# Performance work log

Hardware: AMD Instinct MI355X
Metric: run time of the kernel (lower is better)

The kernel has to match this reference:

```python
import jax, jax.numpy as jnp
import numpy as np

B, A, G, C = 32, 3, 64, 80
MAXB = 50
IOU_THRESH = 0.5


def setup_inputs() -> dict:
    key = jax.random.key(0)
    k1, k2, k3, k4, k5, k6 = jax.random.split(key, 6)
    # predictions hold probabilities directly (log applied in BCE), keep in (0,1)
    predictions = jax.random.uniform(k1, (B, A, G, G, C + 5), jnp.float32, 0.01, 0.99)
    anchors = jnp.concatenate([
        jax.random.uniform(k2, (A, G, G, 2), jnp.float32, 0.0, 512.0),   # cx,cy
        jax.random.uniform(k3, (A, G, G, 2), jnp.float32, 16.0, 160.0),  # w,h
    ], axis=-1)
    cxcy = jax.random.uniform(k4, (B, MAXB, 2), jnp.float32, 0.0, 512.0)
    wh = jax.random.uniform(k5, (B, MAXB, 2), jnp.float32, 16.0, 160.0)
    cls = jax.random.randint(k6, (B, MAXB), 0, C).astype(jnp.float32)
    valid = jax.random.uniform(jax.random.fold_in(key, 7), (B, MAXB)) < 0.6
    cls = jnp.where(valid, cls, -1.0)
    bbox_annotations = jnp.concatenate([cxcy, wh, cls[..., None]], axis=-1)
    return {"predictions": predictions, "bbox_annotations": bbox_annotations,
            "anchors": anchors, "input_dim": 512, "num_classes": C,
            "num_anchors": A, "grid_size": G}


def _iou_xywh(a, b):
    # a: (N,4) (cx,cy,w,h); b: (M,4) -> (N,M) pairwise IoU
    ax1, ay1 = a[:, 0] - a[:, 2] / 2, a[:, 1] - a[:, 3] / 2
    ax2, ay2 = a[:, 0] + a[:, 2] / 2, a[:, 1] + a[:, 3] / 2
    bx1, by1 = b[:, 0] - b[:, 2] / 2, b[:, 1] - b[:, 3] / 2
    bx2, by2 = b[:, 0] + b[:, 2] / 2, b[:, 1] + b[:, 3] / 2
    iw = jnp.clip(jnp.minimum(ax2[:, None], bx2[None, :]) - jnp.maximum(ax1[:, None], bx1[None, :]), 0)
    ih = jnp.clip(jnp.minimum(ay2[:, None], by2[None, :]) - jnp.maximum(ay1[:, None], by1[None, :]), 0)
    inter = iw * ih
    area_a = (ax2 - ax1) * (ay2 - ay1)
    area_b = (bx2 - bx1) * (by2 - by1)
    return inter / jnp.clip(area_a[:, None] + area_b[None, :] - inter, 1e-8)


def _per_image(pred, ann, anchors_flat, num_classes, iou_thresh):
    cls_p = pred[..., 5:].reshape(-1, num_classes)  # (N, C)
    valid = ann[:, 4] != -1                          # (M,)
    ious = _iou_xywh(anchors_flat, ann[:, :4])       # (N, M)
    ious = jnp.where(valid[None, :], ious, -1.0)     # invalid anns never match
    ious_max = ious.max(axis=1)
    ious_argmax = ious.argmax(axis=1)
    positive = ious_max >= iou_thresh                # (N,)
    assigned_cls = jnp.clip(ann[ious_argmax, 4], 0, num_classes - 1).astype(jnp.int32)
    gt = jax.nn.one_hot(assigned_cls, num_classes, dtype=cls_p.dtype) * positive[:, None]
    bce = -(gt * jnp.log(cls_p) + (1.0 - gt) * jnp.log(1.0 - cls_p))
    num_pos = positive.sum()
    cls_loss = (bce * positive[:, None]).sum() / jnp.maximum(num_pos, 1).astype(cls_p.dtype)
    has_ann = valid.any()
    cls_loss = jnp.where(has_ann, cls_loss, 0.0)
    reg_loss = jnp.zeros((), cls_p.dtype)
    return cls_loss, reg_loss


def reference(predictions, bbox_annotations, anchors, input_dim, num_classes, num_anchors, grid_size):
    anchors_flat = anchors.reshape(-1, 4)  # (A*G*G, 4)
    cls_losses, reg_losses = jax.vmap(_per_image, in_axes=(0, 0, None, None, None))(
        predictions, bbox_annotations, anchors_flat, num_classes, IOU_THRESH)
    return jnp.stack([cls_losses, reg_losses])  # (2, B)
```

## Files before the change

### kernel.cpp

```cpp
#include <hip/hip_runtime.h>

#define BATCH   32
#define NCLS    80
#define MAXB    50
#define NANCH   12288
#define BLK     256
#define BLKS_PER_IMG 48
#define ROWLEN  85

__global__ __launch_bounds__(BLK) void yolo_match_bce(
    const float* __restrict__ pred,
    const float* __restrict__ ann,
    const float* __restrict__ anchors,
    float* __restrict__ psum,
    int*   __restrict__ pcnt)
{
    const int blk = blockIdx.x;
    const int b   = blockIdx.y;
    const int n   = blk * BLK + threadIdx.x;

    __shared__ float4 s_box[MAXB];
    __shared__ float  s_area[MAXB];
    __shared__ float  s_cls[MAXB];
    __shared__ int    s_nv;

    if (threadIdx.x < 64) {
        const int lane = threadIdx.x;
        float cx = 0, cy = 0, w = 0, h = 0, cl = -1.0f;
        if (lane < MAXB) {
            const float* a = ann + ((size_t)b * MAXB + lane) * 5;
            cx = a[0]; cy = a[1]; w = a[2]; h = a[3]; cl = a[4];
        }
        const bool valid = (lane < MAXB) && (cl != -1.0f);
        const unsigned long long mask = __ballot(valid);
        if (valid) {
            const int cidx = __popcll(mask & ((1ull << lane) - 1ull));
            const float x1 = cx - w * 0.5f, y1 = cy - h * 0.5f;
            const float x2 = cx + w * 0.5f, y2 = cy + h * 0.5f;
            s_box[cidx]  = make_float4(x1, y1, x2, y2);
            s_area[cidx] = (x2 - x1) * (y2 - y1);
            s_cls[cidx]  = cl;
        }
        if (lane == 0) s_nv = __popcll(mask);
    }
    __syncthreads();

    const float4 a4 = *reinterpret_cast<const float4*>(anchors + (size_t)n * 4);
    const float ax1 = a4.x - a4.z * 0.5f, ay1 = a4.y - a4.w * 0.5f;
    const float ax2 = a4.x + a4.z * 0.5f, ay2 = a4.y + a4.w * 0.5f;
    const float area_a = (ax2 - ax1) * (ay2 - ay1);

    const int nv = s_nv;
    float best = 0.0f;
    int   bestm = 0;
    #pragma unroll 5
    for (int m = 0; m < nv; ++m) {
        const float4 bb = s_box[m];
        float iw = fminf(ax2, bb.z) - fmaxf(ax1, bb.x); iw = fmaxf(iw, 0.0f);
        float ih = fminf(ay2, bb.w) - fmaxf(ay1, bb.y); ih = fmaxf(ih, 0.0f);
        const float inter = iw * ih;
        const float ua    = area_a + s_area[m] - inter;
        const float iou   = inter * __builtin_amdgcn_rcpf(ua);
        if (iou > best) { best = iou; bestm = m; }
    }

    const bool positive = (best >= 0.5f);
    float local = 0.0f;
    if (positive) {
        const int ac = (int)fminf(fmaxf(s_cls[bestm], 0.0f), (float)(NCLS - 1));
        const float* prow = pred + ((size_t)b * NANCH + n) * ROWLEN + 5;
        float S = 0.0f;
        #pragma unroll
        for (int ch = 0; ch < 5; ++ch) {
            float prod = 1.0f;
            #pragma unroll
            for (int j = 0; j < 16; ++j) {
                const float p = prow[ch * 16 + j];
                prod = __builtin_fmaf(-p, prod, prod);
            }
            S += __logf(prod);
        }
        const float pa = prow[ac];
        local = -__logf(pa) + __logf(1.0f - pa) - S;
    }

    float v = local;
    int   c = positive ? 1 : 0;
    #pragma unroll
    for (int off = 32; off > 0; off >>= 1) {
        v += __shfl_down(v, off, 64);
        c += __shfl_down(c, off, 64);
    }
    __shared__ float s_sum[BLK / 64];
    __shared__ int   s_cnt[BLK / 64];
    const int wave = threadIdx.x >> 6;
    if ((threadIdx.x & 63) == 0) { s_sum[wave] = v; s_cnt[wave] = c; }
    __syncthreads();
    if (threadIdx.x == 0) {
        float t = 0.0f; int tc = 0;
        #pragma unroll
        for (int w = 0; w < BLK / 64; ++w) { t += s_sum[w]; tc += s_cnt[w]; }
        psum[b * BLKS_PER_IMG + blk] = t;
        pcnt[b * BLKS_PER_IMG + blk] = tc;
    }
}

__global__ __launch_bounds__(64) void yolo_finalize(
    const float* __restrict__ psum,
    const int*   __restrict__ pcnt,
    float* __restrict__ out)
{
    const int b = blockIdx.x;
    const int t = threadIdx.x;
    float v = (t < BLKS_PER_IMG) ? psum[b * BLKS_PER_IMG + t] : 0.0f;
    int   c = (t < BLKS_PER_IMG) ? pcnt[b * BLKS_PER_IMG + t] : 0;
    #pragma unroll
    for (int off = 32; off > 0; off >>= 1) {
        v += __shfl_down(v, off, 64);
        c += __shfl_down(c, off, 64);
    }
    if (t == 0) {
        const int np = (c > 1) ? c : 1;
        out[b]         = v / (float)np;
        out[BATCH + b] = 0.0f;
    }
}

extern "C" void kernel_launch(void* const* d_in, const int* in_sizes, int n_in,
                              void* d_out, int out_size, void* d_ws, size_t ws_size,
                              hipStream_t stream) {
    const float* pred    = (const float*)d_in[0];
    const float* ann     = (const float*)d_in[1];
    const float* anchors = (const float*)d_in[2];
    float* out = (float*)d_out;

    float* psum = (float*)d_ws;
    int*   pcnt = (int*)((char*)d_ws + sizeof(float) * BATCH * BLKS_PER_IMG);

    dim3 grid1(BLKS_PER_IMG, BATCH);
    yolo_match_bce<<<grid1, BLK, 0, stream>>>(pred, ann, anchors, psum, pcnt);
    yolo_finalize<<<BATCH, 64, 0, stream>>>(psum, pcnt, out);
}
```

Measured before the change: 17.50 us.

## Fuse finalize into main kernel via packed atomic last-block reduction, two anchors per thread

Removes the separate finalize kernel. Each block atomically adds a packed 64-bit word holding a block counter, positive count and fixed-point sum, and the last block writes the per-image loss. Each thread now handles two anchors, which halves the grid and amortizes the shared annotation setup. In exchange it adds a memset launch and converts the sum to fixed point, which can lose precision or overflow the 44-bit field for large losses.

```diff
diff --git a/kernel.cpp b/kernel.cpp
--- a/kernel.cpp
+++ b/kernel.cpp
@@ -5,19 +5,23 @@
 #define MAXB    50
 #define NANCH   12288
 #define BLK     256
-#define BLKS_PER_IMG 48
+#define APT     2
+#define BLKS_PER_IMG (NANCH / (BLK * APT))
 #define ROWLEN  85
+#define SUM_SCALE 16384.0f
 
-__global__ __launch_bounds__(BLK) void yolo_match_bce(
+typedef unsigned long long u64;
+
+__global__ __launch_bounds__(BLK) void yolo_fused(
     const float* __restrict__ pred,
     const float* __restrict__ ann,
     const float* __restrict__ anchors,
-    float* __restrict__ psum,
-    int*   __restrict__ pcnt)
+    u64*         __restrict__ gpack,
+    float*       __restrict__ out)
 {
     const int blk = blockIdx.x;
     const int b   = blockIdx.y;
-    const int n   = blk * BLK + threadIdx.x;
+    const int n0  = blk * (BLK * APT) + threadIdx.x;
 
     __shared__ float4 s_box[MAXB];
     __shared__ float  s_area[MAXB];
@@ -32,7 +36,7 @@
             cx = a[0]; cy = a[1]; w = a[2]; h = a[3]; cl = a[4];
         }
         const bool valid = (lane < MAXB) && (cl != -1.0f);
-        const unsigned long long mask = __ballot(valid);
+        const u64 mask = __ballot(valid);
         if (valid) {
             const int cidx = __popcll(mask & ((1ull << lane) - 1ull));
             const float x1 = cx - w * 0.5f, y1 = cy - h * 0.5f;
@@ -45,47 +49,71 @@
     }
     __syncthreads();
 
-    const float4 a4 = *reinterpret_cast<const float4*>(anchors + (size_t)n * 4);
-    const float ax1 = a4.x - a4.z * 0.5f, ay1 = a4.y - a4.w * 0.5f;
-    const float ax2 = a4.x + a4.z * 0.5f, ay2 = a4.y + a4.w * 0.5f;
-    const float area_a = (ax2 - ax1) * (ay2 - ay1);
+    const float4 A0 = *reinterpret_cast<const float4*>(anchors + (size_t)n0 * 4);
+    const float4 A1 = *reinterpret_cast<const float4*>(anchors + (size_t)(n0 + BLK) * 4);
+    const float ax1_0 = A0.x - A0.z * 0.5f, ay1_0 = A0.y - A0.w * 0.5f;
+    const float ax2_0 = A0.x + A0.z * 0.5f, ay2_0 = A0.y + A0.w * 0.5f;
+    const float ax1_1 = A1.x - A1.z * 0.5f, ay1_1 = A1.y - A1.w * 0.5f;
+    const float ax2_1 = A1.x + A1.z * 0.5f, ay2_1 = A1.y + A1.w * 0.5f;
+    const float area0 = (ax2_0 - ax1_0) * (ay2_0 - ay1_0);
+    const float area1 = (ax2_1 - ax1_1) * (ay2_1 - ay1_1);
 
     const int nv = s_nv;
-    float best = 0.0f;
-    int   bestm = 0;
-    #pragma unroll 5
+    float best0 = 0.0f, best1 = 0.0f;
+    int   bm0 = 0, bm1 = 0;
+    #pragma unroll 2
     for (int m = 0; m < nv; ++m) {
         const float4 bb = s_box[m];
-        float iw = fminf(ax2, bb.z) - fmaxf(ax1, bb.x); iw = fmaxf(iw, 0.0f);
-        float ih = fminf(ay2, bb.w) - fmaxf(ay1, bb.y); ih = fmaxf(ih, 0.0f);
-        const float inter = iw * ih;
-        const float ua    = area_a + s_area[m] - inter;
-        const float iou   = inter * __builtin_amdgcn_rcpf(ua);
-        if (iou > best) { best = iou; bestm = m; }
+        const float ab  = s_area[m];
+        float iw0 = fminf(ax2_0, bb.z) - fmaxf(ax1_0, bb.x); iw0 = fmaxf(iw0, 0.0f);
+        float ih0 = fminf(ay2_0, bb.w) - fmaxf(ay1_0, bb.y); ih0 = fmaxf(ih0, 0.0f);
+        float iw1 = fminf(ax2_1, bb.z) - fmaxf(ax1_1, bb.x); iw1 = fmaxf(iw1, 0.0f);
+        float ih1 = fminf(ay2_1, bb.w) - fmaxf(ay1_1, bb.y); ih1 = fmaxf(ih1, 0.0f);
+        const float in0 = iw0 * ih0;
+        const float in1 = iw1 * ih1;
+        const float iou0 = in0 * __builtin_amdgcn_rcpf(area0 + ab - in0);
+        const float iou1 = in1 * __builtin_amdgcn_rcpf(area1 + ab - in1);
+        if (iou0 > best0) { best0 = iou0; bm0 = m; }
+        if (iou1 > best1) { best1 = iou1; bm1 = m; }
     }
 
-    const bool positive = (best >= 0.5f);
+    const bool pos0 = (best0 >= 0.5f);
+    const bool pos1 = (best1 >= 0.5f);
     float local = 0.0f;
-    if (positive) {
-        const int ac = (int)fminf(fmaxf(s_cls[bestm], 0.0f), (float)(NCLS - 1));
-        const float* prow = pred + ((size_t)b * NANCH + n) * ROWLEN + 5;
+
+    if (pos0) {
+        const int ac = (int)fminf(fmaxf(s_cls[bm0], 0.0f), (float)(NCLS - 1));
+        const float* prow = pred + ((size_t)b * NANCH + n0) * ROWLEN + 5;
         float S = 0.0f;
         #pragma unroll
         for (int ch = 0; ch < 5; ++ch) {
             float prod = 1.0f;
             #pragma unroll
-            for (int j = 0; j < 16; ++j) {
-                const float p = prow[ch * 16 + j];
-                prod = __builtin_fmaf(-p, prod, prod);
-            }
+            for (int j = 0; j < 16; ++j)
+                prod = __builtin_fmaf(-prow[ch * 16 + j], prod, prod);
             S += __logf(prod);
         }
         const float pa = prow[ac];
-        local = -__logf(pa) + __logf(1.0f - pa) - S;
+        local += -__logf(pa) + __logf(1.0f - pa) - S;
+    }
+    if (pos1) {
+        const int ac = (int)fminf(fmaxf(s_cls[bm1], 0.0f), (float)(NCLS - 1));
+        const float* prow = pred + ((size_t)b * NANCH + n0 + BLK) * ROWLEN + 5;
+        float S = 0.0f;
+        #pragma unroll
+        for (int ch = 0; ch < 5; ++ch) {
+            float prod = 1.0f;
+            #pragma unroll
+            for (int j = 0; j < 16; ++j)
+                prod = __builtin_fmaf(-prow[ch * 16 + j], prod, prod);
+            S += __logf(prod);
+        }
+        const float pa = prow[ac];
+        local += -__logf(pa) + __logf(1.0f - pa) - S;
     }
 
     float v = local;
-    int   c = positive ? 1 : 0;
+    int   c = (pos0 ? 1 : 0) + (pos1 ? 1 : 0);
     #pragma unroll
     for (int off = 32; off > 0; off >>= 1) {
         v += __shfl_down(v, off, 64);
@@ -96,33 +124,21 @@
     const int wave = threadIdx.x >> 6;
     if ((threadIdx.x & 63) == 0) { s_sum[wave] = v; s_cnt[wave] = c; }
     __syncthreads();
+
     if (threadIdx.x == 0) {
         float t = 0.0f; int tc = 0;
         #pragma unroll
         for (int w = 0; w < BLK / 64; ++w) { t += s_sum[w]; tc += s_cnt[w]; }
-        psum[b * BLKS_PER_IMG + blk] = t;
-        pcnt[b * BLKS_PER_IMG + blk] = tc;
-    }
-}
-
-__global__ __launch_bounds__(64) void yolo_finalize(
-    const float* __restrict__ psum,
-    const int*   __restrict__ pcnt,
-    float* __restrict__ out)
-{
-    const int b = blockIdx.x;
-    const int t = threadIdx.x;
-    float v = (t < BLKS_PER_IMG) ? psum[b * BLKS_PER_IMG + t] : 0.0f;
-    int   c = (t < BLKS_PER_IMG) ? pcnt[b * BLKS_PER_IMG + t] : 0;
-    #pragma unroll
-    for (int off = 32; off > 0; off >>= 1) {
-        v += __shfl_down(v, off, 64);
-        c += __shfl_down(c, off, 64);
-    }
-    if (t == 0) {
-        const int np = (c > 1) ? c : 1;
-        out[b]         = v / (float)np;
-        out[BATCH + b] = 0.0f;
+        const u64 pack = (1ull << 58) | ((u64)tc << 44)
+                       | (u64)__float2ll_rn(t * SUM_SCALE);
+        const u64 old = atomicAdd(&gpack[b], pack);
+        if ((old >> 58) == (u64)(BLKS_PER_IMG - 1)) {
+            const u64 tot = old + pack;
+            const u64 cnt = (tot >> 44) & 0x3FFFull;
+            const float sum = (float)(tot & ((1ull << 44) - 1ull)) * (1.0f / SUM_SCALE);
+            out[b]         = sum / fmaxf((float)cnt, 1.0f);
+            out[BATCH + b] = 0.0f;
+        }
     }
 }
 
@@ -134,10 +150,9 @@
     const float* anchors = (const float*)d_in[2];
     float* out = (float*)d_out;
 
-    float* psum = (float*)d_ws;
-    int*   pcnt = (int*)((char*)d_ws + sizeof(float) * BATCH * BLKS_PER_IMG);
+    u64* gpack = (u64*)d_ws;
+    (void)hipMemsetAsync(gpack, 0, sizeof(u64) * BATCH, stream);
 
-    dim3 grid1(BLKS_PER_IMG, BATCH);
-    yolo_match_bce<<<grid1, BLK, 0, stream>>>(pred, ann, anchors, psum, pcnt);
-    yolo_finalize<<<BATCH, 64, 0, stream>>>(psum, pcnt, out);
+    dim3 grid(BLKS_PER_IMG, BATCH);
+    yolo_fused<<<grid, BLK, 0, stream>>>(pred, ann, anchors, gpack, out);
 }
```

Measured after the change: 21.99 us. 25.7% more time.

## Process positive anchors wave-cooperatively with coalesced row loads

Applied to the files above, without the earlier changes.

Replaces the per-thread loop over a positive anchor's 80 class probabilities with a loop over the wave's positive anchors. All 64 lanes load one prediction row together, which gives coalesced loads and spreads the log work across lanes. This removes strided per-thread row reads and the divergence caused by scattered positives. In exchange it serializes positives within a wave and calls one log per element instead of using the product trick.

```diff
diff --git a/kernel.cpp b/kernel.cpp
--- a/kernel.cpp
+++ b/kernel.cpp
@@ -8,6 +8,8 @@
 #define BLKS_PER_IMG 48
 #define ROWLEN  85
 
+typedef unsigned long long u64;
+
 __global__ __launch_bounds__(BLK) void yolo_match_bce(
     const float* __restrict__ pred,
     const float* __restrict__ ann,
@@ -15,9 +17,10 @@
     float* __restrict__ psum,
     int*   __restrict__ pcnt)
 {
-    const int blk = blockIdx.x;
-    const int b   = blockIdx.y;
-    const int n   = blk * BLK + threadIdx.x;
+    const int blk  = blockIdx.x;
+    const int b    = blockIdx.y;
+    const int n    = blk * BLK + threadIdx.x;
+    const int lane = threadIdx.x & 63;
 
     __shared__ float4 s_box[MAXB];
     __shared__ float  s_area[MAXB];
@@ -25,23 +28,22 @@
     __shared__ int    s_nv;
 
     if (threadIdx.x < 64) {
-        const int lane = threadIdx.x;
         float cx = 0, cy = 0, w = 0, h = 0, cl = -1.0f;
-        if (lane < MAXB) {
-            const float* a = ann + ((size_t)b * MAXB + lane) * 5;
+        if (threadIdx.x < MAXB) {
+            const float* a = ann + ((size_t)b * MAXB + threadIdx.x) * 5;
             cx = a[0]; cy = a[1]; w = a[2]; h = a[3]; cl = a[4];
         }
-        const bool valid = (lane < MAXB) && (cl != -1.0f);
-        const unsigned long long mask = __ballot(valid);
+        const bool valid = (threadIdx.x < MAXB) && (cl != -1.0f);
+        const u64 mask = __ballot(valid);
         if (valid) {
-            const int cidx = __popcll(mask & ((1ull << lane) - 1ull));
+            const int cidx = __popcll(mask & ((1ull << threadIdx.x) - 1ull));
             const float x1 = cx - w * 0.5f, y1 = cy - h * 0.5f;
             const float x2 = cx + w * 0.5f, y2 = cy + h * 0.5f;
             s_box[cidx]  = make_float4(x1, y1, x2, y2);
             s_area[cidx] = (x2 - x1) * (y2 - y1);
             s_cls[cidx]  = cl;
         }
-        if (lane == 0) s_nv = __popcll(mask);
+        if (threadIdx.x == 0) s_nv = __popcll(mask);
     }
     __syncthreads();
 
@@ -65,23 +67,25 @@
     }
 
     const bool positive = (best >= 0.5f);
+    const int ac = (int)fminf(fmaxf(s_cls[bestm], 0.0f), (float)(NCLS - 1));
+
     float local = 0.0f;
-    if (positive) {
-        const int ac = (int)fminf(fmaxf(s_cls[bestm], 0.0f), (float)(NCLS - 1));
-        const float* prow = pred + ((size_t)b * NANCH + n) * ROWLEN + 5;
-        float S = 0.0f;
-        #pragma unroll
-        for (int ch = 0; ch < 5; ++ch) {
-            float prod = 1.0f;
-            #pragma unroll
-            for (int j = 0; j < 16; ++j) {
-                const float p = prow[ch * 16 + j];
-                prod = __builtin_fmaf(-p, prod, prod);
-            }
-            S += __logf(prod);
-        }
-        const float pa = prow[ac];
-        local = -__logf(pa) + __logf(1.0f - pa) - S;
+    u64 pmask = __ballot(positive);
+    const size_t waverow = (size_t)b * NANCH + (size_t)(n - lane);
+    while (pmask) {
+        const int src = __ffsll(pmask) - 1;
+        pmask &= pmask - 1;
+        const int pac = __shfl(ac, src);
+        const float* prow = pred + (waverow + (size_t)src) * ROWLEN + 5;
+        const float p0 = prow[lane];
+        const float p1 = (lane < 16) ? prow[64 + lane] : 0.0f;
+        float t = __logf(1.0f - p0);
+        if (lane < 16) t += __logf(1.0f - p1);
+        local -= t;
+        const int   tl = (pac < 64) ? pac : (pac - 64);
+        const float pv = (pac < 64) ? p0 : p1;
+        if (lane == tl)
+            local += -__logf(pv) + __logf(1.0f - pv);
     }
 
     float v = local;
```

Measured after the change: 19.39 us. 10.8% more time.

## Fuse finalize into main kernel via packed 64-bit atomic last-block reduction

Applied to the files above, without the earlier changes.

Removes the separate finalize kernel. Each block packs a completion counter, its positive count and a fixed-point scaled partial sum into one 64-bit word and atomically adds it to a per-image accumulator. The block that sees the counter reach the last value computes the mean and writes the output. A memset is added to zero the accumulators. The fixed-point quantization changes rounding, and the packing risks overflow if per-image sums exceed the 44-bit field.

```diff
diff --git a/kernel.cpp b/kernel.cpp
--- a/kernel.cpp
+++ b/kernel.cpp
@@ -7,13 +7,16 @@
 #define BLK     256
 #define BLKS_PER_IMG 48
 #define ROWLEN  85
+#define SUM_SCALE 16384.0f
 
-__global__ __launch_bounds__(BLK) void yolo_match_bce(
+typedef unsigned long long u64;
+
+__global__ __launch_bounds__(BLK) void yolo_fused(
     const float* __restrict__ pred,
     const float* __restrict__ ann,
     const float* __restrict__ anchors,
-    float* __restrict__ psum,
-    int*   __restrict__ pcnt)
+    u64*         __restrict__ gpack,
+    float*       __restrict__ out)
 {
     const int blk = blockIdx.x;
     const int b   = blockIdx.y;
@@ -32,7 +35,7 @@
             cx = a[0]; cy = a[1]; w = a[2]; h = a[3]; cl = a[4];
         }
         const bool valid = (lane < MAXB) && (cl != -1.0f);
-        const unsigned long long mask = __ballot(valid);
+        const u64 mask = __ballot(valid);
         if (valid) {
             const int cidx = __popcll(mask & ((1ull << lane) - 1ull));
             const float x1 = cx - w * 0.5f, y1 = cy - h * 0.5f;
@@ -96,33 +99,21 @@
     const int wave = threadIdx.x >> 6;
     if ((threadIdx.x & 63) == 0) { s_sum[wave] = v; s_cnt[wave] = c; }
     __syncthreads();
+
     if (threadIdx.x == 0) {
         float t = 0.0f; int tc = 0;
         #pragma unroll
         for (int w = 0; w < BLK / 64; ++w) { t += s_sum[w]; tc += s_cnt[w]; }
-        psum[b * BLKS_PER_IMG + blk] = t;
-        pcnt[b * BLKS_PER_IMG + blk] = tc;
-    }
-}
-
-__global__ __launch_bounds__(64) void yolo_finalize(
-    const float* __restrict__ psum,
-    const int*   __restrict__ pcnt,
-    float* __restrict__ out)
-{
-    const int b = blockIdx.x;
-    const int t = threadIdx.x;
-    float v = (t < BLKS_PER_IMG) ? psum[b * BLKS_PER_IMG + t] : 0.0f;
-    int   c = (t < BLKS_PER_IMG) ? pcnt[b * BLKS_PER_IMG + t] : 0;
-    #pragma unroll
-    for (int off = 32; off > 0; off >>= 1) {
-        v += __shfl_down(v, off, 64);
-        c += __shfl_down(c, off, 64);
-    }
-    if (t == 0) {
-        const int np = (c > 1) ? c : 1;
-        out[b]         = v / (float)np;
-        out[BATCH + b] = 0.0f;
+        const u64 pack = (1ull << 58) | ((u64)tc << 44)
+                       | (u64)__float2ll_rn(t * SUM_SCALE);
+        const u64 old = atomicAdd(&gpack[b], pack);
+        if ((old >> 58) == (u64)(BLKS_PER_IMG - 1)) {
+            const u64 tot = old + pack;
+            const u64 cnt = (tot >> 44) & 0x3FFFull;
+            const float sum = (float)(tot & ((1ull << 44) - 1ull)) * (1.0f / SUM_SCALE);
+            out[b]         = sum / fmaxf((float)cnt, 1.0f);
+            out[BATCH + b] = 0.0f;
+        }
     }
 }
 
@@ -134,10 +125,9 @@
     const float* anchors = (const float*)d_in[2];
     float* out = (float*)d_out;
 
-    float* psum = (float*)d_ws;
-    int*   pcnt = (int*)((char*)d_ws + sizeof(float) * BATCH * BLKS_PER_IMG);
+    u64* gpack = (u64*)d_ws;
+    (void)hipMemsetAsync(gpack, 0, sizeof(u64) * BATCH, stream);
 
-    dim3 grid1(BLKS_PER_IMG, BATCH);
-    yolo_match_bce<<<grid1, BLK, 0, stream>>>(pred, ann, anchors, psum, pcnt);
-    yolo_finalize<<<BATCH, 64, 0, stream>>>(psum, pcnt, out);
+    dim3 grid(BLKS_PER_IMG, BATCH);
+    yolo_fused<<<grid, BLK, 0, stream>>>(pred, ann, anchors, gpack, out);
 }
```

Measured after the change: 25.83 us. +47.6%, slower.
